# Performance work log

Measured on AMD Instinct MI355X. Metric: run time of the kernel, lower is better.

The kernel has to match this reference:

```python
import jax, jax.numpy as jnp
import numpy as np

B, S, HIDDEN = 2, 2048, 2048
H, KVH, HD = 16, 4, 128
N_REP = H // KVH
WIN = 3  # hardcoded window_size in the module
ROPE_THETA = 10000.0


def _rope(x, cos, sin):
    # x: [b, s, h, d]; cos/sin: [s, d//2]. Pairs are consecutive elements
    # (view_as_complex on reshape(..., -1, 2)): a = even idx, b = odd idx.
    a = x[..., 0::2]
    b = x[..., 1::2]
    c = cos[None, :, None, :]
    s = sin[None, :, None, :]
    out = jnp.stack([a * c - b * s, a * s + b * c], axis=-1)  # [b,s,h,d//2,2]
    return out.reshape(x.shape)


def setup_inputs() -> dict:
    key = jax.random.key(0)
    ks = jax.random.split(key, 5)
    x = jax.random.normal(ks[0], (B, S, HIDDEN), dtype=jnp.float32)
    scale = 0.02
    wq = jax.random.normal(ks[1], (HIDDEN, H * HD), dtype=jnp.float32) * scale
    wk = jax.random.normal(ks[2], (HIDDEN, KVH * HD), dtype=jnp.float32) * scale
    wv = jax.random.normal(ks[3], (HIDDEN, KVH * HD), dtype=jnp.float32) * scale
    wo = jax.random.normal(ks[4], (H * HD, HIDDEN), dtype=jnp.float32) * scale
    # Standard RoPE angles (equivalent to the complex freqs_cis)
    inv_freq = 1.0 / (ROPE_THETA ** (np.arange(0, HD, 2, dtype=np.float64) / HD))
    ang = np.outer(np.arange(S, dtype=np.float64), inv_freq)  # [S, HD//2]
    cos = jnp.asarray(np.cos(ang), dtype=jnp.float32)
    sin = jnp.asarray(np.sin(ang), dtype=jnp.float32)
    return {"x": x, "wq": wq, "wk": wk, "wv": wv, "wo": wo, "cos": cos, "sin": sin}


def reference(x, wq, wk, wv, wo, cos, sin):
    q = (x @ wq).reshape(B, S, H, HD)
    k = (x @ wk).reshape(B, S, KVH, HD)
    v = (x @ wv).reshape(B, S, KVH, HD)
    q = _rope(q, cos, sin)
    k = _rope(k, cos, sin)
    # GQA: repeat kv heads (repeat_kv)
    k = jnp.repeat(k, N_REP, axis=2)  # [B,S,H,HD]
    v = jnp.repeat(v, N_REP, axis=2)
    scores = jnp.einsum("bqhd,bkhd->bhqk", q, k) / np.float32(np.sqrt(HD))
    i = jnp.arange(S)[:, None]
    j = jnp.arange(S)[None, :]
    allowed = (j <= i) & (j > i - WIN)
    scores = jnp.where(allowed, scores, -jnp.inf)
    attn = jax.nn.softmax(scores.astype(jnp.float32), axis=-1).astype(q.dtype)
    out = jnp.einsum("bhqk,bkhd->bqhd", attn, v).reshape(B, S, H * HD)
    return (out @ wo, attn)
```

## Files before the change

kernel.cpp:

```cpp
#include <hip/hip_runtime.h>

#define SEQ 2048
#define HID 2048
#define NH 16
#define NKVH 4
#define HDIM 128
#define NB 2
#define MTOT (NB * SEQ)
#define QKV_N (NH * HDIM + 2 * NKVH * HDIM)
#define OUT0_ELEMS (NB * SEQ * HID)
#define ATTN_ELEMS ((size_t)NB * NH * SEQ * SEQ)
#define Z1_CHUNK 26048
#define Z1_TOTAL ((long)768 * Z1_CHUNK)
#define Z2_CHUNK 26464

typedef __bf16 bf16x8 __attribute__((ext_vector_type(8)));
typedef float f32x4 __attribute__((ext_vector_type(4)));

__device__ __forceinline__ unsigned short f2bf(float f) {
  unsigned int u = __float_as_uint(f);
  u += 0x7FFFu + ((u >> 16) & 1u);
  return (unsigned short)(u >> 16);
}
__device__ __forceinline__ float bf2f(unsigned short u) {
  return __uint_as_float(((unsigned int)u) << 16);
}

__global__ __launch_bounds__(256) void prep_k(
    const float* __restrict__ x, const float* __restrict__ wq,
    const float* __restrict__ wk, const float* __restrict__ wv,
    const float* __restrict__ wo, unsigned short* __restrict__ Xbf,
    unsigned short* __restrict__ Wqkvt, unsigned short* __restrict__ Wot) {
  __shared__ float tile[32][33];
  const int bid = blockIdx.x, t = threadIdx.x;
  if (bid < 8192) {
    int i = bid * 256 + t;
    float4 v = ((const float4*)x)[i];
    ushort4 o;
    o.x = f2bf(v.x); o.y = f2bf(v.y); o.z = f2bf(v.z); o.w = f2bf(v.w);
    ((ushort4*)Xbf)[i] = o;
    return;
  }
  int lb = bid - 8192;
  const float* W; unsigned short* Wt; int gx, N;
  if (lb < 4096)      { W = wq; Wt = Wqkvt;                       gx = 64; N = 2048; }
  else if (lb < 5120) { W = wk; Wt = Wqkvt + (size_t)2048 * HID;  gx = 16; N = 512;  lb -= 4096; }
  else if (lb < 6144) { W = wv; Wt = Wqkvt + (size_t)2560 * HID;  gx = 16; N = 512;  lb -= 5120; }
  else                { W = wo; Wt = Wot;                         gx = 64; N = 2048; lb -= 6144; }
  const int n0 = (lb % gx) * 32, k0 = (lb / gx) * 32;
  const int tx = t & 31, ty = t >> 5;
  #pragma unroll
  for (int r = 0; r < 32; r += 8)
    tile[ty + r][tx] = W[(size_t)(k0 + ty + r) * N + n0 + tx];
  __syncthreads();
  #pragma unroll
  for (int r = 0; r < 32; r += 8)
    Wt[(size_t)(n0 + ty + r) * HID + k0 + tx] = f2bf(tile[tx][ty + r]);
}

template <bool OUT_BF16>
__global__ __launch_bounds__(256) void gemm_bt_k(
    const unsigned short* __restrict__ A, const unsigned short* __restrict__ Bt,
    void* __restrict__ Cv, int M, int N, int K,
    f32x4* __restrict__ attn4, long zoff, int zchunk) {
  __shared__ unsigned short As[128 * 32];
  __shared__ unsigned short Bs[128 * 32];
  const int t = threadIdx.x;
  const int nbx = gridDim.x;
  const int rawbid = blockIdx.y * nbx + blockIdx.x;
  const int nwg = nbx * gridDim.y;
  const int sw = (rawbid & 7) * (nwg >> 3) + (rawbid >> 3);
  const int row0 = (sw / nbx) << 7;
  const int col0 = (sw % nbx) << 7;
  const int lane = t & 63;
  const int wave = t >> 6;
  const int wr = (wave >> 1) << 6;
  const int wc = (wave & 1) << 6;
  const int lrow = lane & 15;
  const int kofs = (lane >> 4) << 3;

  const long zbase = zoff + (long)rawbid * zchunk;

  f32x4 acc[4][4];
  #pragma unroll
  for (int a = 0; a < 4; ++a)
    #pragma unroll
    for (int b = 0; b < 4; ++b)
      #pragma unroll
      for (int r = 0; r < 4; ++r) acc[a][b][r] = 0.f;

  const int ar0 = t >> 2, ac0 = (t & 3) << 3;
  const int ar1 = ar0 + 64;

  const unsigned short* Ab = A + (size_t)row0 * K;
  const unsigned short* Bb = Bt + (size_t)col0 * K;

  const int nk = K >> 5;
  for (int kt = 0; kt < nk; ++kt) {
    const int k0 = kt << 5;
    if (kt) __syncthreads();
    __builtin_amdgcn_global_load_lds(
        (const __attribute__((address_space(1))) void*)(Ab + (size_t)ar0 * K + k0 + ac0),
        (__attribute__((address_space(3))) void*)(As + t * 8), 16, 0, 0);
    __builtin_amdgcn_global_load_lds(
        (const __attribute__((address_space(1))) void*)(Ab + (size_t)ar1 * K + k0 + ac0),
        (__attribute__((address_space(3))) void*)(As + (t + 256) * 8), 16, 0, 0);
    __builtin_amdgcn_global_load_lds(
        (const __attribute__((address_space(1))) void*)(Bb + (size_t)ar0 * K + k0 + ac0),
        (__attribute__((address_space(3))) void*)(Bs + t * 8), 16, 0, 0);
    __builtin_amdgcn_global_load_lds(
        (const __attribute__((address_space(1))) void*)(Bb + (size_t)ar1 * K + k0 + ac0),
        (__attribute__((address_space(3))) void*)(Bs + (t + 256) * 8), 16, 0, 0);
    __syncthreads();

    bf16x8 af[4], bfr[4];
    #pragma unroll
    for (int mf = 0; mf < 4; ++mf)
      af[mf] = *(const bf16x8*)(As + ((wr + mf * 16 + lrow) << 5) + kofs);
    #pragma unroll
    for (int nf = 0; nf < 4; ++nf)
      bfr[nf] = *(const bf16x8*)(Bs + ((wc + nf * 16 + lrow) << 5) + kofs);

    #pragma unroll
    for (int s = 0; s < 2; ++s) {
      int il = (kt * 2 + s) * 256 + t;
      if (il < zchunk) {
        long g = zbase + il;
        int c = (int)(g & 511);
        int i = (int)((g >> 9) & (SEQ - 1));
        int hi = i >> 2;
        int lo = (i >= 2 ? i - 2 : 0) >> 2;
        if (c != hi && c != lo) {
          f32x4 z = {0.f, 0.f, 0.f, 0.f};
          __builtin_nontemporal_store(z, attn4 + g);
        }
      }
    }

    #pragma unroll
    for (int mf = 0; mf < 4; ++mf)
      #pragma unroll
      for (int nf = 0; nf < 4; ++nf)
        acc[mf][nf] = __builtin_amdgcn_mfma_f32_16x16x32_bf16(af[mf], bfr[nf],
                                                              acc[mf][nf], 0, 0, 0);
  }

  const int cr = row0 + wr + ((lane >> 4) << 2);
  const int cc = col0 + wc + (lane & 15);
  #pragma unroll
  for (int mf = 0; mf < 4; ++mf)
    #pragma unroll
    for (int nf = 0; nf < 4; ++nf)
      #pragma unroll
      for (int r = 0; r < 4; ++r) {
        size_t idx = (size_t)(cr + mf * 16 + r) * N + cc + nf * 16;
        if constexpr (OUT_BF16)
          ((unsigned short*)Cv)[idx] = f2bf(acc[mf][nf][r]);
        else
          ((float*)Cv)[idx] = acc[mf][nf][r];
      }
}

__device__ __forceinline__ float rope_val(float v, int lane, float c, float s) {
  float p = __shfl_xor(v, 1, 64);
  return (lane & 1) ? (p * s + v * c) : (v * c - p * s);
}

__global__ void attn_k(const unsigned short* __restrict__ QKV,
                       unsigned short* __restrict__ AO,
                       float* __restrict__ attn_out,
                       const float* __restrict__ cosT,
                       const float* __restrict__ sinT) {
  int unit = blockIdx.x * 4 + (threadIdx.x >> 6);
  int lane = threadIdx.x & 63;
  int h = unit & (NH - 1);
  int mi = unit >> 4;
  int i = mi & (SEQ - 1);
  int kh = h >> 2;
  const float SCALE = 0.08838834764831845f;
  const int tt = lane >> 1;

  const unsigned short* qp = QKV + (size_t)mi * QKV_N + h * HDIM;
  float ci0 = cosT[i * 64 + tt],      si0 = sinT[i * 64 + tt];
  float ci1 = cosT[i * 64 + 32 + tt], si1 = sinT[i * 64 + 32 + tt];
  float q0 = rope_val(bf2f(qp[lane]),      lane, ci0, si0);
  float q1 = rope_val(bf2f(qp[lane + 64]), lane, ci1, si1);

  float sc[3];
  #pragma unroll
  for (int jj = 0; jj < 3; ++jj) {
    int j = i - 2 + jj;
    float d = -1e30f;
    if (j >= 0) {
      const unsigned short* kp = QKV + (size_t)(mi - i + j) * QKV_N + 2048 + kh * HDIM;
      float cj0 = cosT[j * 64 + tt],      sj0 = sinT[j * 64 + tt];
      float cj1 = cosT[j * 64 + 32 + tt], sj1 = sinT[j * 64 + 32 + tt];
      float k0 = rope_val(bf2f(kp[lane]),      lane, cj0, sj0);
      float k1 = rope_val(bf2f(kp[lane + 64]), lane, cj1, sj1);
      float part = q0 * k0 + q1 * k1;
      #pragma unroll
      for (int o = 32; o; o >>= 1) part += __shfl_xor(part, o, 64);
      d = part * SCALE;
    }
    sc[jj] = d;
  }
  float mx = fmaxf(fmaxf(sc[0], sc[1]), sc[2]);
  float p0 = __expf(sc[0] - mx), p1 = __expf(sc[1] - mx), p2 = __expf(sc[2] - mx);
  float inv = 1.0f / (p0 + p1 + p2);
  float aw[3] = {p0 * inv, p1 * inv, p2 * inv};

  float o0 = 0.f, o1 = 0.f;
  #pragma unroll
  for (int jj = 0; jj < 3; ++jj) {
    int j = i - 2 + jj;
    if (j >= 0) {
      const unsigned short* vp = QKV + (size_t)(mi - i + j) * QKV_N + 2560 + kh * HDIM;
      o0 += aw[jj] * bf2f(vp[lane]);
      o1 += aw[jj] * bf2f(vp[lane + 64]);
    }
  }
  size_t ao_base = (size_t)mi * HID + h * HDIM;
  AO[ao_base + lane] = f2bf(o0);
  AO[ao_base + lane + 64] = f2bf(o1);

  int b = mi >> 11;
  int rowg = (b * NH + h) * SEQ + i;
  int lo = (i >= 2 ? i - 2 : 0) >> 2;
  int hi = i >> 2;
  if (lane == 0 || (lane == 1 && hi != lo)) {
    int c = (lane == 0) ? lo : hi;
    f32x4 val = {0.f, 0.f, 0.f, 0.f};
    #pragma unroll
    for (int q = 0; q < 4; ++q) {
      int j = c * 4 + q;
      int d = j - (i - 2);
      if (d >= 0 && d < 3 && j <= i) val[q] = aw[d];
    }
    __builtin_nontemporal_store(val, (f32x4*)(attn_out + (size_t)rowg * SEQ) + c);
  }
}

extern "C" void kernel_launch(void* const* d_in, const int* in_sizes, int n_in,
                              void* d_out, int out_size, void* d_ws, size_t ws_size,
                              hipStream_t stream) {
  const float* x    = (const float*)d_in[0];
  const float* wq   = (const float*)d_in[1];
  const float* wk   = (const float*)d_in[2];
  const float* wv   = (const float*)d_in[3];
  const float* wo   = (const float*)d_in[4];
  const float* cosT = (const float*)d_in[5];
  const float* sinT = (const float*)d_in[6];

  float* out  = (float*)d_out;
  float* attn = out + OUT0_ELEMS;

  char* ws = (char*)d_ws;
  unsigned short* Xbf   = (unsigned short*)ws;  ws += (size_t)MTOT * HID * 2;
  unsigned short* Wqkvt = (unsigned short*)ws;  ws += (size_t)QKV_N * HID * 2;
  unsigned short* Wot   = (unsigned short*)ws;  ws += (size_t)HID * HID * 2;
  unsigned short* QKV   = (unsigned short*)ws;  ws += (size_t)MTOT * QKV_N * 2;
  unsigned short* AO    = (unsigned short*)ws;

  prep_k<<<18432, 256, 0, stream>>>(x, wq, wk, wv, wo, Xbf, Wqkvt, Wot);

  gemm_bt_k<true><<<dim3(QKV_N / 128, MTOT / 128), 256, 0, stream>>>(
      Xbf, Wqkvt, QKV, MTOT, QKV_N, HID, (f32x4*)attn, 0L, Z1_CHUNK);

  attn_k<<<MTOT * NH / 4, 256, 0, stream>>>(QKV, AO, attn, cosT, sinT);

  gemm_bt_k<false><<<dim3(HID / 128, MTOT / 128), 256, 0, stream>>>(
      AO, Wot, out, MTOT, HID, HID, (f32x4*)attn, Z1_TOTAL, Z2_CHUNK);
}
```

Baseline: 197.3 us.

## Double GEMM K-tile to 64 and share KV across GQA heads in attention

```diff
diff --git a/kernel.cpp b/kernel.cpp
--- a/kernel.cpp
+++ b/kernel.cpp
@@ -63,8 +63,8 @@
     const unsigned short* __restrict__ A, const unsigned short* __restrict__ Bt,
     void* __restrict__ Cv, int M, int N, int K,
     f32x4* __restrict__ attn4, long zoff, int zchunk) {
-  __shared__ unsigned short As[128 * 32];
-  __shared__ unsigned short Bs[128 * 32];
+  __shared__ unsigned short As[128 * 64];
+  __shared__ unsigned short Bs[128 * 64];
   const int t = threadIdx.x;
   const int nbx = gridDim.x;
   const int rawbid = blockIdx.y * nbx + blockIdx.x;
@@ -89,41 +89,29 @@
       #pragma unroll
       for (int r = 0; r < 4; ++r) acc[a][b][r] = 0.f;
 
-  const int ar0 = t >> 2, ac0 = (t & 3) << 3;
-  const int ar1 = ar0 + 64;
-
   const unsigned short* Ab = A + (size_t)row0 * K;
   const unsigned short* Bb = Bt + (size_t)col0 * K;
 
-  const int nk = K >> 5;
+  const int nk = K >> 6;
   for (int kt = 0; kt < nk; ++kt) {
-    const int k0 = kt << 5;
+    const int k0 = kt << 6;
     if (kt) __syncthreads();
-    __builtin_amdgcn_global_load_lds(
-        (const __attribute__((address_space(1))) void*)(Ab + (size_t)ar0 * K + k0 + ac0),
-        (__attribute__((address_space(3))) void*)(As + t * 8), 16, 0, 0);
-    __builtin_amdgcn_global_load_lds(
-        (const __attribute__((address_space(1))) void*)(Ab + (size_t)ar1 * K + k0 + ac0),
-        (__attribute__((address_space(3))) void*)(As + (t + 256) * 8), 16, 0, 0);
-    __builtin_amdgcn_global_load_lds(
-        (const __attribute__((address_space(1))) void*)(Bb + (size_t)ar0 * K + k0 + ac0),
-        (__attribute__((address_space(3))) void*)(Bs + t * 8), 16, 0, 0);
-    __builtin_amdgcn_global_load_lds(
-        (const __attribute__((address_space(1))) void*)(Bb + (size_t)ar1 * K + k0 + ac0),
-        (__attribute__((address_space(3))) void*)(Bs + (t + 256) * 8), 16, 0, 0);
+    #pragma unroll
+    for (int i = 0; i < 4; ++i) {
+      const int c = i * 256 + t;
+      const int row = c >> 3, c8 = (c & 7) << 3;
+      __builtin_amdgcn_global_load_lds(
+          (const __attribute__((address_space(1))) void*)(Ab + (size_t)row * K + k0 + c8),
+          (__attribute__((address_space(3))) void*)(As + c * 8), 16, 0, 0);
+      __builtin_amdgcn_global_load_lds(
+          (const __attribute__((address_space(1))) void*)(Bb + (size_t)row * K + k0 + c8),
+          (__attribute__((address_space(3))) void*)(Bs + c * 8), 16, 0, 0);
+    }
     __syncthreads();
 
-    bf16x8 af[4], bfr[4];
-    #pragma unroll
-    for (int mf = 0; mf < 4; ++mf)
-      af[mf] = *(const bf16x8*)(As + ((wr + mf * 16 + lrow) << 5) + kofs);
-    #pragma unroll
-    for (int nf = 0; nf < 4; ++nf)
-      bfr[nf] = *(const bf16x8*)(Bs + ((wc + nf * 16 + lrow) << 5) + kofs);
-
-    #pragma unroll
-    for (int s = 0; s < 2; ++s) {
-      int il = (kt * 2 + s) * 256 + t;
+    #pragma unroll
+    for (int s = 0; s < 4; ++s) {
+      int il = (kt * 4 + s) * 256 + t;
       if (il < zchunk) {
         long g = zbase + il;
         int c = (int)(g & 511);
@@ -138,11 +126,21 @@
     }
 
     #pragma unroll
-    for (int mf = 0; mf < 4; ++mf)
+    for (int ks = 0; ks < 2; ++ks) {
+      bf16x8 af[4], bfr[4];
+      #pragma unroll
+      for (int mf = 0; mf < 4; ++mf)
+        af[mf] = *(const bf16x8*)(As + ((wr + mf * 16 + lrow) << 6) + (ks << 5) + kofs);
       #pragma unroll
       for (int nf = 0; nf < 4; ++nf)
-        acc[mf][nf] = __builtin_amdgcn_mfma_f32_16x16x32_bf16(af[mf], bfr[nf],
-                                                              acc[mf][nf], 0, 0, 0);
+        bfr[nf] = *(const bf16x8*)(Bs + ((wc + nf * 16 + lrow) << 6) + (ks << 5) + kofs);
+      #pragma unroll
+      for (int mf = 0; mf < 4; ++mf)
+        #pragma unroll
+        for (int nf = 0; nf < 4; ++nf)
+          acc[mf][nf] = __builtin_amdgcn_mfma_f32_16x16x32_bf16(af[mf], bfr[nf],
+                                                                acc[mf][nf], 0, 0, 0);
+    }
   }
 
   const int cr = row0 + wr + ((lane >> 4) << 2);
@@ -161,11 +159,6 @@
       }
 }
 
-__device__ __forceinline__ float rope_val(float v, int lane, float c, float s) {
-  float p = __shfl_xor(v, 1, 64);
-  return (lane & 1) ? (p * s + v * c) : (v * c - p * s);
-}
-
 __global__ void attn_k(const unsigned short* __restrict__ QKV,
                        unsigned short* __restrict__ AO,
                        float* __restrict__ attn_out,
@@ -173,70 +166,81 @@
                        const float* __restrict__ sinT) {
   int unit = blockIdx.x * 4 + (threadIdx.x >> 6);
   int lane = threadIdx.x & 63;
-  int h = unit & (NH - 1);
-  int mi = unit >> 4;
+  int kh = unit & (NKVH - 1);
+  int mi = unit >> 2;
   int i = mi & (SEQ - 1);
-  int kh = h >> 2;
+  int b = mi >> 11;
   const float SCALE = 0.08838834764831845f;
-  const int tt = lane >> 1;
-
-  const unsigned short* qp = QKV + (size_t)mi * QKV_N + h * HDIM;
-  float ci0 = cosT[i * 64 + tt],      si0 = sinT[i * 64 + tt];
-  float ci1 = cosT[i * 64 + 32 + tt], si1 = sinT[i * 64 + 32 + tt];
-  float q0 = rope_val(bf2f(qp[lane]),      lane, ci0, si0);
-  float q1 = rope_val(bf2f(qp[lane + 64]), lane, ci1, si1);
-
-  float sc[3];
-  #pragma unroll
-  for (int jj = 0; jj < 3; ++jj) {
-    int j = i - 2 + jj;
-    float d = -1e30f;
-    if (j >= 0) {
-      const unsigned short* kp = QKV + (size_t)(mi - i + j) * QKV_N + 2048 + kh * HDIM;
-      float cj0 = cosT[j * 64 + tt],      sj0 = sinT[j * 64 + tt];
-      float cj1 = cosT[j * 64 + 32 + tt], sj1 = sinT[j * 64 + 32 + tt];
-      float k0 = rope_val(bf2f(kp[lane]),      lane, cj0, sj0);
-      float k1 = rope_val(bf2f(kp[lane + 64]), lane, cj1, sj1);
-      float part = q0 * k0 + q1 * k1;
-      #pragma unroll
-      for (int o = 32; o; o >>= 1) part += __shfl_xor(part, o, 64);
-      d = part * SCALE;
-    }
-    sc[jj] = d;
-  }
-  float mx = fmaxf(fmaxf(sc[0], sc[1]), sc[2]);
-  float p0 = __expf(sc[0] - mx), p1 = __expf(sc[1] - mx), p2 = __expf(sc[2] - mx);
-  float inv = 1.0f / (p0 + p1 + p2);
-  float aw[3] = {p0 * inv, p1 * inv, p2 * inv};
-
-  float o0 = 0.f, o1 = 0.f;
+
+  float ci = cosT[i * 64 + lane], si = sinT[i * 64 + lane];
+
+  float qa[4], qb[4];
+  #pragma unroll
+  for (int hh = 0; hh < 4; ++hh) {
+    ushort2 qv = *(const ushort2*)(QKV + (size_t)mi * QKV_N + (kh * 4 + hh) * HDIM + 2 * lane);
+    float a = bf2f(qv.x), bb = bf2f(qv.y);
+    qa[hh] = a * ci - bb * si;
+    qb[hh] = a * si + bb * ci;
+  }
+
+  float ka[3], kb[3], va[3], vb[3];
+  #pragma unroll
+  for (int jj = 0; jj < 3; ++jj) { ka[jj] = kb[jj] = va[jj] = vb[jj] = 0.f; }
   #pragma unroll
   for (int jj = 0; jj < 3; ++jj) {
     int j = i - 2 + jj;
     if (j >= 0) {
-      const unsigned short* vp = QKV + (size_t)(mi - i + j) * QKV_N + 2560 + kh * HDIM;
-      o0 += aw[jj] * bf2f(vp[lane]);
-      o1 += aw[jj] * bf2f(vp[lane + 64]);
-    }
-  }
-  size_t ao_base = (size_t)mi * HID + h * HDIM;
-  AO[ao_base + lane] = f2bf(o0);
-  AO[ao_base + lane + 64] = f2bf(o1);
-
-  int b = mi >> 11;
-  int rowg = (b * NH + h) * SEQ + i;
+      const unsigned short* rp = QKV + (size_t)(mi - i + j) * QKV_N;
+      float cj = cosT[j * 64 + lane], sj = sinT[j * 64 + lane];
+      ushort2 kv = *(const ushort2*)(rp + 2048 + kh * HDIM + 2 * lane);
+      float a = bf2f(kv.x), bb = bf2f(kv.y);
+      ka[jj] = a * cj - bb * sj;
+      kb[jj] = a * sj + bb * cj;
+      ushort2 vv = *(const ushort2*)(rp + 2560 + kh * HDIM + 2 * lane);
+      va[jj] = bf2f(vv.x); vb[jj] = bf2f(vv.y);
+    }
+  }
+
+  float d[4][3];
+  #pragma unroll
+  for (int hh = 0; hh < 4; ++hh)
+    #pragma unroll
+    for (int jj = 0; jj < 3; ++jj) {
+      int j = i - 2 + jj;
+      float part = qa[hh] * ka[jj] + qb[hh] * kb[jj];
+      #pragma unroll
+      for (int o = 32; o; o >>= 1) part += __shfl_xor(part, o, 64);
+      d[hh][jj] = (j >= 0) ? part * SCALE : -1e30f;
+    }
+
+  int rowb = (b * NH + kh * 4) * SEQ + i;
   int lo = (i >= 2 ? i - 2 : 0) >> 2;
   int hi = i >> 2;
-  if (lane == 0 || (lane == 1 && hi != lo)) {
-    int c = (lane == 0) ? lo : hi;
-    f32x4 val = {0.f, 0.f, 0.f, 0.f};
-    #pragma unroll
-    for (int q = 0; q < 4; ++q) {
-      int j = c * 4 + q;
-      int d = j - (i - 2);
-      if (d >= 0 && d < 3 && j <= i) val[q] = aw[d];
-    }
-    __builtin_nontemporal_store(val, (f32x4*)(attn_out + (size_t)rowg * SEQ) + c);
+  #pragma unroll
+  for (int hh = 0; hh < 4; ++hh) {
+    float mx = fmaxf(fmaxf(d[hh][0], d[hh][1]), d[hh][2]);
+    float p0 = __expf(d[hh][0] - mx), p1 = __expf(d[hh][1] - mx), p2 = __expf(d[hh][2] - mx);
+    float inv = 1.0f / (p0 + p1 + p2);
+    float aw0 = p0 * inv, aw1 = p1 * inv, aw2 = p2 * inv;
+
+    float oa = aw0 * va[0] + aw1 * va[1] + aw2 * va[2];
+    float ob = aw0 * vb[0] + aw1 * vb[1] + aw2 * vb[2];
+    ushort2 ov; ov.x = f2bf(oa); ov.y = f2bf(ob);
+    *(ushort2*)(AO + (size_t)mi * HID + (kh * 4 + hh) * HDIM + 2 * lane) = ov;
+
+    if (lane == 2 * hh || (lane == 2 * hh + 1 && hi != lo)) {
+      int c = (lane == 2 * hh) ? lo : hi;
+      f32x4 val = {0.f, 0.f, 0.f, 0.f};
+      float aw[3] = {aw0, aw1, aw2};
+      #pragma unroll
+      for (int q = 0; q < 4; ++q) {
+        int j = c * 4 + q;
+        int dd = j - (i - 2);
+        if (dd >= 0 && dd < 3 && j <= i) val[q] = aw[dd];
+      }
+      __builtin_nontemporal_store(
+          val, (f32x4*)(attn_out + ((size_t)rowb + (size_t)hh * SEQ) * SEQ) + c);
+    }
   }
 }
 
@@ -266,7 +270,7 @@
   gemm_bt_k<true><<<dim3(QKV_N / 128, MTOT / 128), 256, 0, stream>>>(
       Xbf, Wqkvt, QKV, MTOT, QKV_N, HID, (f32x4*)attn, 0L, Z1_CHUNK);
 
-  attn_k<<<MTOT * NH / 4, 256, 0, stream>>>(QKV, AO, attn, cosT, sinT);
+  attn_k<<<MTOT * NKVH / 4, 256, 0, stream>>>(QKV, AO, attn, cosT, sinT);
 
   gemm_bt_k<false><<<dim3(HID / 128, MTOT / 128), 256, 0, stream>>>(
       AO, Wot, out, MTOT, HID, HID, (f32x4*)attn, Z1_TOTAL, Z2_CHUNK);
```

Result: faster. 188.6 us, median of 2 (-4.4%).
